# Kernel optimization log

Hardware: AMD Instinct MI355X
Metric: run time of the kernel (lower is better)

Reference implementation:

```python
import jax, jax.numpy as jnp
import numpy as np

B, D, H, E, W, R = 2048, 1024, 2048, 16, 4, 8
SCALE = 1.0


def setup_inputs() -> dict:
    key = jax.random.key(0)
    ks = jax.random.split(key, 10)
    s = 0.02
    return dict(
        z=jax.random.normal(ks[0], (B, D), jnp.float32),
        top_k=2,
        capacity=256,
        ban_expert=-1,
        tau=jnp.float32(1.0),
        epsilon=jnp.float32(0.0),
        fc1_w=jax.random.uniform(ks[1], (H, D), jnp.float32, -1.0, 1.0) / np.sqrt(D),
        fc1_b=jnp.zeros((H,), jnp.float32),
        fc2_w=jax.random.uniform(ks[2], (D, H), jnp.float32, -1.0, 1.0) / np.sqrt(H),
        fc2_b=jnp.zeros((D,), jnp.float32),
        prototypes=s * jax.random.normal(ks[3], (E, D), jnp.float32),
        adapter_keys=s * jax.random.normal(ks[4], (E, W, D), jnp.float32),
        expert_bias=jnp.zeros((E,), jnp.float32),
        a1=s * jax.random.normal(ks[5], (E, W, R, D), jnp.float32),
        b1=s * jax.random.normal(ks[6], (E, W, H, R), jnp.float32),
        a2=s * jax.random.normal(ks[7], (E, W, R, H), jnp.float32),
        b2=s * jax.random.normal(ks[8], (E, W, D, R), jnp.float32),
    )


def capacity_route(probs, top_k, capacity):
    # Greedy, order-dependent capacity-limited top-k routing (faithful to the
    # Python double loop): tokens processed in order, each takes its highest-
    # prob candidates whose expert still has free capacity.
    Bn, En = probs.shape
    k = min(top_k, En)
    cand_k = min(En, max(4 * k, k))
    cap_limit = max(1, capacity)
    vals, idxs = jax.lax.top_k(probs, cand_k)  # [B, cand_k]

    def token_step(cap, row):
        v_row, i_row = row

        def cand_step(st, x):
            slot, cap, a_idx, a_w, hit = st
            v, e, j = x
            take = (slot < k) & (cap[e] < cap_limit)
            s = jnp.minimum(slot, k - 1)
            a_idx = a_idx.at[s].set(jnp.where(take, e, a_idx[s]))
            a_w = a_w.at[s].set(jnp.where(take, v, a_w[s]))
            cap = cap.at[e].add(jnp.where(take, 1, 0).astype(cap.dtype))
            hit = hit + jnp.where(take & (j > 0), 1, 0)
            slot = slot + jnp.where(take, 1, 0)
            return (slot, cap, a_idx, a_w, hit), None

        init = (jnp.int32(0), cap,
                jnp.full((k,), -1, jnp.int32),
                jnp.zeros((k,), probs.dtype),
                jnp.int32(0))
        (slot, cap, a_idx, a_w, hit), _ = jax.lax.scan(
            cand_step, init, (v_row, i_row.astype(jnp.int32), jnp.arange(cand_k)))
        return cap, (a_idx, a_w, hit)

    cap0 = jnp.zeros((En,), jnp.int32)
    _, (assigned_idx, assigned_w, hits) = jax.lax.scan(token_step, cap0, (vals, idxs))
    cap_hit_rate = hits.sum().astype(probs.dtype) / max(1, Bn * k)
    return assigned_idx, assigned_w, cap_hit_rate


def reference(z, top_k, capacity, ban_expert, tau, epsilon,
              fc1_w, fc1_b, fc2_w, fc2_b, prototypes, adapter_keys,
              expert_bias, a1, b1, a2, b2):
    Bn = z.shape[0]
    En = prototypes.shape[0]
    h_pre = jax.nn.silu(z @ fc1_w.T + fc1_b)          # [B, H]
    out_pre = h_pre @ fc2_w.T + fc2_b                 # [B, D]

    logits = (z @ prototypes.T) / jnp.maximum(tau, 1e-6) + expert_bias
    logits = jnp.where(jnp.arange(En)[None, :] == ban_expert, -1e9, logits)
    probs = jax.nn.softmax(logits, axis=-1)
    probs = (1.0 - epsilon) * probs + epsilon / En

    assigned_idx, assigned_w, cap_hit_rate = capacity_route(probs, top_k, capacity)
    k = assigned_idx.shape[1]
    valid = assigned_idx >= 0                          # [B, k]
    e_safe = jnp.where(valid, assigned_idx, 0)         # [B, k]

    # adapter selection: argmax_w  z . adapter_keys[e, w]
    ak = adapter_keys[e_safe]                          # [B, k, W, D]
    a_idx = jnp.argmax(jnp.einsum('bd,bkwd->bkw', z, ak), axis=-1)  # [B, k]

    A1 = a1[e_safe, a_idx]                             # [B, k, R, D]
    B1 = b1[e_safe, a_idx]                             # [B, k, H, R]
    A2 = a2[e_safe, a_idx]                             # [B, k, R, H]
    B2 = b2[e_safe, a_idx]                             # [B, k, D, R]

    t1 = jnp.einsum('bd,bkrd->bkr', z, A1)
    d1 = jnp.einsum('bkr,bkhr->bkh', t1, B1) * SCALE
    h = jax.nn.silu(h_pre[:, None, :] + d1)            # [B, k, H]
    t2 = jnp.einsum('bkh,bkrh->bkr', h, A2)
    d2 = jnp.einsum('bkr,bkdr->bkd', t2, B2) * SCALE
    y = out_pre[:, None, :] + d2                       # [B, k, D]

    w = jnp.where(valid, assigned_w, 0.0)[:, :, None].astype(z.dtype)
    z_out = (w * y).sum(axis=1)                        # [B, D]

    used_mask = jnp.zeros((Bn, En), bool).at[jnp.arange(Bn)[:, None], e_safe].max(valid)
    # event lists, slot-major order, -1 marks unassigned slots (fixed shape for jit)
    ev_e = jnp.where(valid, assigned_idx, -1).T.reshape(-1)
    ev_a = jnp.where(valid, a_idx, -1).T.reshape(-1)

    return (z + z_out, probs, used_mask, assigned_idx, assigned_w,
            cap_hit_rate, ev_e, ev_a)
```

## Files before the change

### kernel.cpp

```cpp
#include <hip/hip_runtime.h>
#include <stdint.h>

#define NTOK 2048
#define DDIM 1024
#define HDIM 2048
#define NEXP 16

#define O_PROBS 2097152
#define O_USED  2129920
#define O_AIDX  2162688
#define O_AW    2166784
#define O_HIT   2170880
#define O_EVE   2170881
#define O_EVA   2174977

static constexpr size_t WS_ZBF    = 0;
static constexpr size_t WS_FC1WBF = WS_ZBF    + (size_t)NTOK * DDIM * 2;
static constexpr size_t WS_FC2WBF = WS_FC1WBF + (size_t)HDIM * DDIM * 2;
static constexpr size_t WS_HPREBF = WS_FC2WBF + (size_t)DDIM * HDIM * 2;
static constexpr size_t WS_OUTPRE = WS_HPREBF + (size_t)NTOK * HDIM * 2;
static constexpr size_t WS_A1BF   = WS_OUTPRE + (size_t)NTOK * DDIM * 4;
static constexpr size_t WS_B1BF   = WS_A1BF   + (size_t)16 * 4 * 8 * 1024 * 2;
static constexpr size_t WS_A2BF   = WS_B1BF   + (size_t)16 * 4 * 2048 * 8 * 2;
static constexpr size_t WS_B2BF   = WS_A2BF   + (size_t)16 * 4 * 8 * 2048 * 2;
static constexpr size_t WS_CANDS  = WS_B2BF   + (size_t)16 * 4 * 1024 * 8 * 2;
static constexpr size_t WS_CVALS  = WS_CANDS  + (size_t)NTOK * 4;
static constexpr size_t WS_ARGPK  = WS_CVALS  + (size_t)NTOK * 8 * 4;
static constexpr size_t WS_ASGN   = WS_ARGPK  + (size_t)NTOK * 4;
static constexpr size_t WS_ASGNW  = WS_ASGN   + (size_t)NTOK * 4;
static constexpr size_t WS_OUTPR2 = WS_ASGNW  + (size_t)NTOK * 2 * 4;
static constexpr size_t WS_TOTAL2 = WS_OUTPR2 + (size_t)NTOK * DDIM * 4;

typedef __bf16 v8bf __attribute__((ext_vector_type(8)));
typedef float v4f __attribute__((ext_vector_type(4)));
typedef unsigned short us8v __attribute__((ext_vector_type(8)));

__device__ __forceinline__ unsigned short f2bf(float f) {
  unsigned u = __float_as_uint(f);
  u = u + 0x7fffu + ((u >> 16) & 1u);
  return (unsigned short)(u >> 16);
}
__device__ __forceinline__ float bf2f(unsigned short s) {
  return __uint_as_float(((unsigned)s) << 16);
}
__device__ __forceinline__ void gload_lds16(const void* g, void* l) {
  __builtin_amdgcn_global_load_lds(
      (const __attribute__((address_space(1))) void*)g,
      (__attribute__((address_space(3))) void*)l, 16, 0, 0);
}
__device__ __forceinline__ float dot4(float4 a, float4 b) {
  return a.x * b.x + a.y * b.y + a.z * b.z + a.w * b.w;
}

__global__ __launch_bounds__(256) void k1_scores(
    const float* __restrict__ z, const float* __restrict__ proto,
    const float* __restrict__ ebias, const float* __restrict__ ak,
    const float* __restrict__ p_tau, const float* __restrict__ p_eps,
    const int* __restrict__ p_ban,
    unsigned short* __restrict__ zbf, float* __restrict__ out,
    unsigned* __restrict__ cands, float* __restrict__ cvals,
    unsigned* __restrict__ argpk,
    const float* __restrict__ fc1w, const float* __restrict__ fc2w,
    const float* __restrict__ a1, const float* __restrict__ b1,
    const float* __restrict__ a2, const float* __restrict__ b2,
    unsigned short* __restrict__ fc1wbf, unsigned short* __restrict__ fc2wbf,
    unsigned short* __restrict__ a1bf, unsigned short* __restrict__ b1bf,
    unsigned short* __restrict__ a2bf, unsigned short* __restrict__ b2bf)
{
  __shared__ float zs[4][DDIM];
  __shared__ float part[80 * 17];
  __shared__ float sc[4 * 80];
  const int tid = threadIdx.x;
  const int tb = blockIdx.x * 4;
#pragma unroll
  for (int i = 0; i < 4; ++i) {
    const int col = tid * 4;
    float4 v = *(const float4*)&z[(size_t)(tb + i) * DDIM + col];
    *(float4*)&zs[i][col] = v;
    ushort4 bv;
    bv.x = f2bf(v.x); bv.y = f2bf(v.y); bv.z = f2bf(v.z); bv.w = f2bf(v.w);
    *(ushort4*)&zbf[(size_t)(tb + i) * DDIM + col] = bv;
  }
  __syncthreads();
  const int wv = tid >> 6, l = tid & 63;

  {
    const float4* akr = (const float4*)(ak + (size_t)l * DDIM + wv * 256);
    const float4* z0 = (const float4*)&zs[0][0] + wv * 64;
    const float4* z1 = (const float4*)&zs[1][0] + wv * 64;
    const float4* z2 = (const float4*)&zs[2][0] + wv * 64;
    const float4* z3 = (const float4*)&zs[3][0] + wv * 64;
    float a0 = 0.f, a1v = 0.f, a2v = 0.f, a3 = 0.f;
#pragma unroll 8
    for (int i = 0; i < 64; ++i) {
      float4 w = akr[i];
      a0 += dot4(z0[i], w); a1v += dot4(z1[i], w);
      a2v += dot4(z2[i], w); a3 += dot4(z3[i], w);
    }
    part[l * 17 + 0 * 4 + wv] = a0;
    part[l * 17 + 1 * 4 + wv] = a1v;
    part[l * 17 + 2 * 4 + wv] = a2v;
    part[l * 17 + 3 * 4 + wv] = a3;
  }
  if (l < 16) {
    const float4* pr = (const float4*)(proto + (size_t)l * DDIM + wv * 256);
    const float4* z0 = (const float4*)&zs[0][0] + wv * 64;
    const float4* z1 = (const float4*)&zs[1][0] + wv * 64;
    const float4* z2 = (const float4*)&zs[2][0] + wv * 64;
    const float4* z3 = (const float4*)&zs[3][0] + wv * 64;
    float a0 = 0.f, a1v = 0.f, a2v = 0.f, a3 = 0.f;
#pragma unroll 8
    for (int i = 0; i < 64; ++i) {
      float4 w = pr[i];
      a0 += dot4(z0[i], w); a1v += dot4(z1[i], w);
      a2v += dot4(z2[i], w); a3 += dot4(z3[i], w);
    }
    part[(64 + l) * 17 + 0 * 4 + wv] = a0;
    part[(64 + l) * 17 + 1 * 4 + wv] = a1v;
    part[(64 + l) * 17 + 2 * 4 + wv] = a2v;
    part[(64 + l) * 17 + 3 * 4 + wv] = a3;
  }
  __syncthreads();
  for (int o = tid; o < 320; o += 256) {
    const int row = o >> 2, tk = o & 3;
    sc[tk * 80 + row] =
        ((part[row * 17 + tk * 4 + 0] + part[row * 17 + tk * 4 + 1]) +
         part[row * 17 + tk * 4 + 2]) + part[row * 17 + tk * 4 + 3];
  }
  __syncthreads();
  if (tid < 4) {
    const int t = tb + tid;
    const float tau = fmaxf(p_tau[0], 1e-6f);
    const float eps = p_eps[0];
    const int ban = p_ban[0];
    float lg[16];
#pragma unroll
    for (int e = 0; e < 16; ++e) {
      float v = sc[tid * 80 + 64 + e] / tau + ebias[e];
      lg[e] = (e == ban) ? -1e9f : v;
    }
    float mx = lg[0];
#pragma unroll
    for (int e = 1; e < 16; ++e) mx = fmaxf(mx, lg[e]);
    float ex[16]; float sm = 0.f;
#pragma unroll
    for (int e = 0; e < 16; ++e) { ex[e] = expf(lg[e] - mx); sm += ex[e]; }
    float p[16];
#pragma unroll
    for (int e = 0; e < 16; ++e) {
      p[e] = (1.f - eps) * (ex[e] / sm) + eps / (float)NEXP;
      out[O_PROBS + (size_t)t * NEXP + e] = p[e];
    }
    unsigned pack = 0, taken = 0;
#pragma unroll
    for (int r = 0; r < 8; ++r) {
      float bv = -1e30f; int bi = 0;
#pragma unroll
      for (int e = 0; e < 16; ++e) {
        const bool c = !((taken >> e) & 1u) && (p[e] > bv);
        bv = c ? p[e] : bv; bi = c ? e : bi;
      }
      taken |= 1u << bi;
      pack |= ((unsigned)bi) << (4 * r);
      cvals[(size_t)t * 8 + r] = bv;
    }
    cands[t] = pack;
    unsigned apk = 0;
#pragma unroll
    for (int e = 0; e < 16; ++e) {
      float b = sc[tid * 80 + e * 4]; int bi = 0;
#pragma unroll
      for (int w = 1; w < 4; ++w) {
        const float v = sc[tid * 80 + e * 4 + w];
        if (v > b) { b = v; bi = w; }
      }
      apk |= ((unsigned)bi) << (2 * e);
    }
    argpk[t] = apk;
  }
  size_t j = (size_t)blockIdx.x * 256 + tid;
  const size_t stride = (size_t)512 * 256;
  for (; j < 1835008ull; j += stride) {
    const float* src; unsigned short* dst; size_t off;
    if (j < 524288) { src = fc1w; dst = fc1wbf; off = j; }
    else if (j < 1048576) { src = fc2w; dst = fc2wbf; off = j - 524288; }
    else if (j < 1179648) { src = a1; dst = a1bf; off = j - 1048576; }
    else if (j < 1441792) { src = b1; dst = b1bf; off = j - 1179648; }
    else if (j < 1703936) { src = a2; dst = a2bf; off = j - 1441792; }
    else { src = b2; dst = b2bf; off = j - 1703936; }
    float4 v = *(const float4*)&src[off * 4];
    ushort4 bv;
    bv.x = f2bf(v.x); bv.y = f2bf(v.y); bv.z = f2bf(v.z); bv.w = f2bf(v.w);
    *(ushort4*)&dst[off * 4] = bv;
  }
}

__device__ __forceinline__ void route_decide(unsigned c, int avail,
                                             unsigned& m, int& dec) {
  unsigned flags = 0;
#pragma unroll
  for (int j = 0; j < 8; ++j) {
    const int e = (c >> (4 * j)) & 15;
    flags |= ((unsigned)(avail >> e) & 1u) << j;
  }
  const int pc = __popc(flags);
  const int sc = pc < 2 ? pc : 2;
  const int j0 = __ffs(flags) - 1;
  const int j1 = __ffs(flags & (flags - 1)) - 1;
  const int r0 = sc > 0 ? j0 : 0;
  const int r1 = sc > 1 ? j1 : 0;
  const int e0 = (c >> (4 * r0)) & 15;
  const int e1 = (c >> (4 * r1)) & 15;
  m = (sc > 0 ? (1u << e0) : 0u) | (sc > 1 ? (1u << e1) : 0u);
  dec = e0 | (e1 << 4) | (r0 << 8) | (r1 << 11) | (sc << 14);
}

struct RouterSm {
  unsigned long long bal[32][17];
  int cap[16], T[16];
  int avail, t0, tfin, done, hits;
};

__global__ __launch_bounds__(1024) void k2_router(
    const unsigned* __restrict__ cands, const float* __restrict__ cvals,
    const unsigned* __restrict__ argpk, const int* __restrict__ p_cap,
    float* __restrict__ out, int* __restrict__ asgn, float* __restrict__ asgnw)
{
  __shared__ RouterSm S;
  const int tid = threadIdx.x;
  const int w = tid >> 6, l = tid & 63;
  if (tid == 0) { S.avail = 0xFFFF; S.t0 = 0; S.done = 0; S.hits = 0; }
  if (tid < 16) S.cap[tid] = 0;
  const int capl = max(1, p_cap[0]);
  const unsigned cA = cands[tid], cB = cands[tid + 1024];
  const unsigned aA = argpk[tid], aB = argpk[tid + 1024];
  int hits = 0;
  __syncthreads();

  for (int round = 0; round < 20; ++round) {
    const int t0 = S.t0;
    const int avail = S.avail;
    unsigned mA = 0, mB = 0;
    int dA = 0, dB = 0;
    if (tid >= t0) route_decide(cA, avail, mA, dA);
    if (tid + 1024 >= t0) route_decide(cB, avail, mB, dB);
    if (w * 64 + 63 < t0) {
      if (l < 16) S.bal[w][l] = 0ull;
    } else {
      for (int av = avail; av; av &= av - 1) {
        const int e = __ffs(av) - 1;
        unsigned long long b = __ballot((mA >> e) & 1);
        if (l == e) S.bal[w][e] = b;
      }
    }
    if (w * 64 + 1024 + 63 < t0) {
      if (l < 16) S.bal[w + 16][l] = 0ull;
    } else {
      for (int av = avail; av; av &= av - 1) {
        const int e = __ffs(av) - 1;
        unsigned long long b = __ballot((mB >> e) & 1);
        if (l == e) S.bal[w + 16][e] = b;
      }
    }
    __syncthreads();
    unsigned long long bm = 0;
    const bool eav = (avail >> w) & 1;
    {
      int myT = 0x7FFFFFFF;
      if (eav) {
        int cnt = 0;
        if (l < 32) { bm = S.bal[l][w]; cnt = __popcll(bm); }
        int tot = cnt;
#pragma unroll
        for (int o = 32; o; o >>= 1) tot += __shfl_xor(tot, o, 64);
        const int rem = capl - S.cap[w];
        if (tot >= rem) {
          int incl = cnt;
#pragma unroll
          for (int o = 1; o < 32; o <<= 1) {
            int u = __shfl_up(incl, o, 64);
            if (l >= o) incl += u;
          }
          if (l < 32) {
            const int need = rem - (incl - cnt);
            if (need >= 1 && need <= cnt) {
              unsigned long long bb = bm;
              for (int i = 1; i < need; ++i) bb &= bb - 1;
              myT = l * 64 + (__ffsll((unsigned long long)bb) - 1);
            }
          }
#pragma unroll
          for (int o = 32; o; o >>= 1) myT = min(myT, __shfl_xor(myT, o, 64));
        }
      }
      if (l == 0) S.T[w] = myT;
    }
    __syncthreads();
    if (w == 0) {
      int v = (l < 16) ? S.T[l] : 0x7FFFFFFF;
      int ts = v;
#pragma unroll
      for (int o = 32; o; o >>= 1) ts = min(ts, __shfl_xor(ts, o, 64));
      const int done = (ts == 0x7FFFFFFF);
      const int tf = done ? (NTOK - 1) : ts;
      if (l == 0) { S.tfin = tf; S.done = done; S.t0 = tf + 1; }
      if (l < 16 && v == ts) atomicAnd(&S.avail, ~(1 << l));
    }
    __syncthreads();
    const int tfin = S.tfin;
    if (eav) {
      int c2 = 0;
      if (l < 32) {
        const int hi = tfin - l * 64;
        unsigned long long mk =
            (hi < 0) ? 0ull : (hi >= 63 ? ~0ull : ((1ull << (hi + 1)) - 1ull));
        c2 = __popcll(bm & mk);
      }
#pragma unroll
      for (int o = 32; o; o >>= 1) c2 += __shfl_xor(c2, o, 64);
      if (l == 0) S.cap[w] += c2;
    }
#pragma unroll
    for (int half = 0; half < 2; ++half) {
      const int t = tid + half * 1024;
      const int d = half ? dB : dA;
      const unsigned ap = half ? aB : aA;
      if (t < t0 || t > tfin) continue;
      const int e0 = d & 15, e1 = (d >> 4) & 15;
      const int r0 = (d >> 8) & 7, r1 = (d >> 11) & 7, sc = (d >> 14) & 3;
      const int a0 = (ap >> (2 * e0)) & 3, a1i = (ap >> (2 * e1)) & 3;
      asgn[t] = e0 | (e1 << 4) | (a0 << 8) | (a1i << 10) | (sc << 12);
      asgnw[t * 2 + 0] = sc > 0 ? cvals[(size_t)t * 8 + r0] : 0.f;
      asgnw[t * 2 + 1] = sc > 1 ? cvals[(size_t)t * 8 + r1] : 0.f;
      hits += (sc > 0 && r0 > 0) + (sc > 1 && r1 > 0);
    }
    __syncthreads();
    if (S.done) break;
  }
#pragma unroll
  for (int o = 32; o; o >>= 1) hits += __shfl_xor(hits, o, 64);
  if (l == 0) atomicAdd(&S.hits, hits);
  __syncthreads();
  if (tid == 0) out[O_HIT] = (float)S.hits / (float)(NTOK * 2);
}

template <int EPI>
__device__ __forceinline__ void gemm_body(
    unsigned short* As, unsigned short* Bs, int bid,
    const unsigned short* __restrict__ A, const unsigned short* __restrict__ Bm,
    const float* __restrict__ bias, void* __restrict__ Cout,
    int M, int N, int Kloop, int lda, int add_bias)
{
  const int tid = threadIdx.x;
  const int wv = tid >> 6, l = tid & 63;
  const int ntile = N >> 7;
  const int trow = (bid / ntile) << 7;
  const int tcol = (bid % ntile) << 7;
  const int wr = wv >> 1, wc = wv & 1;
  v4f acc[4][4];
#pragma unroll
  for (int m = 0; m < 4; ++m)
#pragma unroll
    for (int n = 0; n < 4; ++n) acc[m][n] = (v4f){0.f, 0.f, 0.f, 0.f};

  const int lrow8 = l >> 3;
  const int lcol8 = (l & 7) << 3;
  const unsigned short* gA = A + (size_t)trow * lda;
  const unsigned short* gB = Bm + (size_t)tcol * lda;
  const int fr = l & 15, kof = (l >> 4) << 3;

  for (int k0 = 0; k0 < Kloop; k0 += 64) {
    __syncthreads();
#pragma unroll
    for (int i = 0; i < 4; ++i) {
      const int s = (wv << 2) + i;
      gload_lds16(gA + (size_t)(s * 8 + lrow8) * lda + k0 + lcol8, &As[s * 512]);
      gload_lds16(gB + (size_t)(s * 8 + lrow8) * lda + k0 + lcol8, &Bs[s * 512]);
    }
    __syncthreads();
    v8bf af[4][2], bf[4][2];
#pragma unroll
    for (int m = 0; m < 4; ++m) {
      const int row = wr * 64 + m * 16 + fr;
      af[m][0] = *(const v8bf*)&As[row * 64 + kof];
      af[m][1] = *(const v8bf*)&As[row * 64 + 32 + kof];
    }
#pragma unroll
    for (int n = 0; n < 4; ++n) {
      const int row = wc * 64 + n * 16 + fr;
      bf[n][0] = *(const v8bf*)&Bs[row * 64 + kof];
      bf[n][1] = *(const v8bf*)&Bs[row * 64 + 32 + kof];
    }
#pragma unroll
    for (int ks = 0; ks < 2; ++ks)
#pragma unroll
      for (int m = 0; m < 4; ++m)
#pragma unroll
        for (int n = 0; n < 4; ++n)
          acc[m][n] = __builtin_amdgcn_mfma_f32_16x16x32_bf16(
              af[m][ks], bf[n][ks], acc[m][n], 0, 0, 0);
  }
  const int fq = l >> 4;
#pragma unroll
  for (int m = 0; m < 4; ++m)
#pragma unroll
    for (int n = 0; n < 4; ++n) {
      const int col = tcol + wc * 64 + n * 16 + fr;
      const float bc = add_bias ? bias[col] : 0.f;
#pragma unroll
      for (int j = 0; j < 4; ++j) {
        const int row = trow + wr * 64 + m * 16 + fq * 4 + j;
        const float v = acc[m][n][j] + bc;
        if (EPI == 0) {
          const float sv = v / (1.f + __expf(-v));
          ((unsigned short*)Cout)[(size_t)row * N + col] = f2bf(sv);
        } else {
          ((float*)Cout)[(size_t)row * N + col] = v;
        }
      }
    }
}

__global__ __launch_bounds__(256) void gemm_bt0(
    const unsigned short* __restrict__ A, const unsigned short* __restrict__ Bm,
    const float* __restrict__ bias, void* __restrict__ Cout,
    int M, int N, int K)
{
  __shared__ __align__(16) char smem[32768];
  gemm_body<0>((unsigned short*)smem, (unsigned short*)smem + 8192,
               blockIdx.x, A, Bm, bias, Cout, M, N, K, K, 1);
}

__global__ __launch_bounds__(256) void gemm_bt1s(
    const unsigned short* __restrict__ A, const unsigned short* __restrict__ Bm,
    const float* __restrict__ bias, float* __restrict__ C0,
    float* __restrict__ C1)
{
  __shared__ __align__(16) char smem[32768];
  const int ntiles = (NTOK / 128) * (DDIM / 128);
  const int half = blockIdx.x / ntiles;
  const int tile = blockIdx.x % ntiles;
  gemm_body<1>((unsigned short*)smem, (unsigned short*)smem + 8192,
               tile, A + half * 1024, Bm + half * 1024, bias,
               half ? (void*)C1 : (void*)C0,
               NTOK, DDIM, 1024, HDIM, half == 0);
}

__global__ __launch_bounds__(256) void gemm_bt1f(
    const unsigned short* __restrict__ A, const unsigned short* __restrict__ Bm,
    const float* __restrict__ bias, void* __restrict__ Cout,
    int M, int N, int K)
{
  __shared__ __align__(16) char smem[32768];
  gemm_body<1>((unsigned short*)smem, (unsigned short*)smem + 8192,
               blockIdx.x, A, Bm, bias, Cout, M, N, K, K, 1);
}

__global__ __launch_bounds__(256) void k5_lora(
    const float* __restrict__ z, const unsigned short* __restrict__ hpre,
    const float* __restrict__ outpre, const float* __restrict__ outpre2,
    int use2, const int* __restrict__ asgn, const float* __restrict__ asgnw,
    const unsigned short* __restrict__ a1, const unsigned short* __restrict__ b1,
    const unsigned short* __restrict__ a2, const unsigned short* __restrict__ b2,
    float* __restrict__ out0, float* __restrict__ out)
{
  __shared__ float zl[DDIM];
  __shared__ float hl[HDIM];
  __shared__ float t1s[8], t2s[8];
  const int b = blockIdx.x, tid = threadIdx.x;
  {
    float4 v = *(const float4*)&z[(size_t)b * DDIM + tid * 4];
    *(float4*)&zl[tid * 4] = v;
  }
  const int pk = asgn[b];
  const int sc = (pk >> 12) & 3;
  const int eA0 = pk & 15, eA1 = (pk >> 4) & 15;
  const int aA0 = (pk >> 8) & 3, aA1 = (pk >> 10) & 3;
  const float w0 = asgnw[b * 2 + 0], w1 = asgnw[b * 2 + 1];
  if (tid < 16)
    out[O_USED + (size_t)b * 16 + tid] =
        (float)((sc > 0 && tid == eA0) || (sc > 1 && tid == eA1));
  if (tid == 0) {
    out[O_AIDX + (size_t)b * 2 + 0] = sc > 0 ? (float)eA0 : -1.f;
    out[O_AIDX + (size_t)b * 2 + 1] = sc > 1 ? (float)eA1 : -1.f;
    out[O_AW + (size_t)b * 2 + 0] = w0;
    out[O_AW + (size_t)b * 2 + 1] = w1;
    out[O_EVE + b] = sc > 0 ? (float)eA0 : -1.f;
    out[O_EVE + NTOK + b] = sc > 1 ? (float)eA1 : -1.f;
    out[O_EVA + b] = sc > 0 ? (float)aA0 : -1.f;
    out[O_EVA + NTOK + b] = sc > 1 ? (float)aA1 : -1.f;
  }
  float acc[4] = {0.f, 0.f, 0.f, 0.f};
  float wsum = 0.f;
  const int r = tid >> 5, l5 = tid & 31;
  const float4* zg = (const float4*)&z[(size_t)b * DDIM];
  __syncthreads();

  for (int s = 0; s < 2; ++s) {
    if (s >= sc) continue;
    const float ww = (s == 0) ? w0 : w1;
    const int ad = ((s == 0) ? eA0 : eA1) * 4 + ((s == 0) ? aA0 : aA1);
    wsum += ww;
    {
      const us8v* pa1 = (const us8v*)(a1 + ((size_t)ad * 8 + r) * DDIM);
      float sa = 0.f;
#pragma unroll
      for (int i = 0; i < 4; ++i) {
        const int g = l5 + 32 * i;
        us8v va = pa1[g];
        float4 z0 = zg[g * 2], z1 = zg[g * 2 + 1];
        sa += z0.x * bf2f(va[0]) + z0.y * bf2f(va[1]) +
              z0.z * bf2f(va[2]) + z0.w * bf2f(va[3]) +
              z1.x * bf2f(va[4]) + z1.y * bf2f(va[5]) +
              z1.z * bf2f(va[6]) + z1.w * bf2f(va[7]);
      }
#pragma unroll
      for (int o = 16; o; o >>= 1) sa += __shfl_xor(sa, o, 64);
      if (l5 == 0) t1s[r] = sa;
    }
    __syncthreads();
    {
      float t1r[8];
#pragma unroll
      for (int q = 0; q < 8; ++q) t1r[q] = t1s[q];
      const unsigned short* pb1 = b1 + (size_t)ad * HDIM * 8;
      const unsigned short* ph = hpre + (size_t)b * HDIM;
#pragma unroll
      for (int j = 0; j < 8; ++j) {
        const int hh_i = tid + 256 * j;
        us8v row = *(const us8v*)&pb1[(size_t)hh_i * 8];
        float d1 = 0.f;
#pragma unroll
        for (int q = 0; q < 8; ++q) d1 += t1r[q] * bf2f(row[q]);
        const float hh = bf2f(ph[hh_i]) + d1;
        hl[hh_i] = hh / (1.f + __expf(-hh));
      }
    }
    __syncthreads();
    {
      const us8v* pa2 = (const us8v*)(a2 + ((size_t)ad * 8 + r) * HDIM);
      float sa = 0.f;
#pragma unroll
      for (int i = 0; i < 8; ++i) {
        const int g = l5 + 32 * i;
        us8v va = pa2[g];
        const float* hp = &hl[g * 8];
        sa += hp[0] * bf2f(va[0]) + hp[1] * bf2f(va[1]) +
              hp[2] * bf2f(va[2]) + hp[3] * bf2f(va[3]) +
              hp[4] * bf2f(va[4]) + hp[5] * bf2f(va[5]) +
              hp[6] * bf2f(va[6]) + hp[7] * bf2f(va[7]);
      }
#pragma unroll
      for (int o = 16; o; o >>= 1) sa += __shfl_xor(sa, o, 64);
      if (l5 == 0) t2s[r] = sa;
    }
    __syncthreads();
    {
      float t2r[8];
#pragma unroll
      for (int q = 0; q < 8; ++q) t2r[q] = t2s[q];
      const unsigned short* pb2 = b2 + (size_t)ad * DDIM * 8;
#pragma unroll
      for (int j = 0; j < 4; ++j) {
        const int d = tid + 256 * j;
        us8v row = *(const us8v*)&pb2[(size_t)d * 8];
        float d2 = 0.f;
#pragma unroll
        for (int q = 0; q < 8; ++q) d2 += t2r[q] * bf2f(row[q]);
        acc[j] += ww * d2;
      }
    }
    __syncthreads();
  }
#pragma unroll
  for (int j = 0; j < 4; ++j) {
    const int d = tid + 256 * j;
    float op = outpre[(size_t)b * DDIM + d];
    if (use2) op += outpre2[(size_t)b * DDIM + d];
    out0[(size_t)b * DDIM + d] = zl[d] + wsum * op + acc[j];
  }
}

extern "C" void kernel_launch(void* const* d_in, const int* in_sizes, int n_in,
                              void* d_out, int out_size, void* d_ws, size_t ws_size,
                              hipStream_t stream)
{
  (void)in_sizes; (void)n_in; (void)out_size;
  const float* z     = (const float*)d_in[0];
  const int*   p_cap = (const int*)d_in[2];
  const int*   p_ban = (const int*)d_in[3];
  const float* p_tau = (const float*)d_in[4];
  const float* p_eps = (const float*)d_in[5];
  const float* fc1w  = (const float*)d_in[6];
  const float* fc1b  = (const float*)d_in[7];
  const float* fc2w  = (const float*)d_in[8];
  const float* fc2b  = (const float*)d_in[9];
  const float* proto = (const float*)d_in[10];
  const float* ak    = (const float*)d_in[11];
  const float* ebias = (const float*)d_in[12];
  const float* a1    = (const float*)d_in[13];
  const float* b1    = (const float*)d_in[14];
  const float* a2    = (const float*)d_in[15];
  const float* b2    = (const float*)d_in[16];
  float* out = (float*)d_out;
  char* ws = (char*)d_ws;

  unsigned short* zbf    = (unsigned short*)(ws + WS_ZBF);
  unsigned short* fc1wbf = (unsigned short*)(ws + WS_FC1WBF);
  unsigned short* fc2wbf = (unsigned short*)(ws + WS_FC2WBF);
  unsigned short* hprebf = (unsigned short*)(ws + WS_HPREBF);
  float*          outpre = (float*)(ws + WS_OUTPRE);
  unsigned short* a1bf   = (unsigned short*)(ws + WS_A1BF);
  unsigned short* b1bf   = (unsigned short*)(ws + WS_B1BF);
  unsigned short* a2bf   = (unsigned short*)(ws + WS_A2BF);
  unsigned short* b2bf   = (unsigned short*)(ws + WS_B2BF);
  unsigned*       cands  = (unsigned*)(ws + WS_CANDS);
  float*          cvals  = (float*)(ws + WS_CVALS);
  unsigned*       argpk  = (unsigned*)(ws + WS_ARGPK);
  int*            asgn   = (int*)(ws + WS_ASGN);
  float*          asgnw  = (float*)(ws + WS_ASGNW);
  float*          outpr2 = (float*)(ws + WS_OUTPR2);
  const int splitk = (ws_size >= WS_TOTAL2) ? 1 : 0;

  k1_scores<<<512, 256, 0, stream>>>(
      z, proto, ebias, ak, p_tau, p_eps, p_ban, zbf, out, cands, cvals, argpk,
      fc1w, fc2w, a1, b1, a2, b2, fc1wbf, fc2wbf, a1bf, b1bf, a2bf, b2bf);

  k2_router<<<1, 1024, 0, stream>>>(
      cands, cvals, argpk, p_cap, out, asgn, asgnw);

  gemm_bt0<<<(NTOK / 128) * (HDIM / 128), 256, 0, stream>>>(
      zbf, fc1wbf, fc1b, (void*)hprebf, NTOK, HDIM, DDIM);

  if (splitk) {
    gemm_bt1s<<<2 * (NTOK / 128) * (DDIM / 128), 256, 0, stream>>>(
        hprebf, fc2wbf, fc2b, outpre, outpr2);
  } else {
    gemm_bt1f<<<(NTOK / 128) * (DDIM / 128), 256, 0, stream>>>(
        hprebf, fc2wbf, fc2b, (void*)outpre, NTOK, DDIM, HDIM);
  }

  k5_lora<<<NTOK, 256, 0, stream>>>(
      z, hprebf, outpre, outpr2, splitk, asgn, asgnw,
      a1bf, b1bf, a2bf, b2bf, out, out);
}
```

Measured before the change: 279.5 us.

## Overlap weight bf16 conversion with serial router and trim router barriers

Moves the fp32-to-bf16 conversion of the fc and LoRA weights out of the scoring kernel into extra blocks of the single-block router launch, so the conversion runs on otherwise idle CUs while the serial routing loop executes. The router itself keeps capacity, avail and t0 in registers, double-buffers the ballot array, and drops one barrier per round by having every wave compute the min threshold redundantly. It also preloads candidate values into registers. The risk is that the conversion blocks contend for memory bandwidth with the router block, and the conversion loop now runs with a different block count.

```diff
diff --git a/kernel.cpp b/kernel.cpp
--- a/kernel.cpp
+++ b/kernel.cpp
@@ -59,13 +59,7 @@
     const int* __restrict__ p_ban,
     unsigned short* __restrict__ zbf, float* __restrict__ out,
     unsigned* __restrict__ cands, float* __restrict__ cvals,
-    unsigned* __restrict__ argpk,
-    const float* __restrict__ fc1w, const float* __restrict__ fc2w,
-    const float* __restrict__ a1, const float* __restrict__ b1,
-    const float* __restrict__ a2, const float* __restrict__ b2,
-    unsigned short* __restrict__ fc1wbf, unsigned short* __restrict__ fc2wbf,
-    unsigned short* __restrict__ a1bf, unsigned short* __restrict__ b1bf,
-    unsigned short* __restrict__ a2bf, unsigned short* __restrict__ b2bf)
+    unsigned* __restrict__ argpk)
 {
   __shared__ float zs[4][DDIM];
   __shared__ float part[80 * 17];
@@ -178,22 +172,9 @@
     }
     argpk[t] = apk;
   }
-  size_t j = (size_t)blockIdx.x * 256 + tid;
-  const size_t stride = (size_t)512 * 256;
-  for (; j < 1835008ull; j += stride) {
-    const float* src; unsigned short* dst; size_t off;
-    if (j < 524288) { src = fc1w; dst = fc1wbf; off = j; }
-    else if (j < 1048576) { src = fc2w; dst = fc2wbf; off = j - 524288; }
-    else if (j < 1179648) { src = a1; dst = a1bf; off = j - 1048576; }
-    else if (j < 1441792) { src = b1; dst = b1bf; off = j - 1179648; }
-    else if (j < 1703936) { src = a2; dst = a2bf; off = j - 1441792; }
-    else { src = b2; dst = b2bf; off = j - 1703936; }
-    float4 v = *(const float4*)&src[off * 4];
-    ushort4 bv;
-    bv.x = f2bf(v.x); bv.y = f2bf(v.y); bv.z = f2bf(v.z); bv.w = f2bf(v.w);
-    *(ushort4*)&dst[off * 4] = bv;
-  }
-}
+}
+
+#define CONVB 224
 
 __device__ __forceinline__ void route_decide(unsigned c, int avail,
                                              unsigned& m, int& dec) {
@@ -215,99 +196,107 @@
   dec = e0 | (e1 << 4) | (r0 << 8) | (r1 << 11) | (sc << 14);
 }
 
-struct RouterSm {
-  unsigned long long bal[32][17];
-  int cap[16], T[16];
-  int avail, t0, tfin, done, hits;
-};
-
-__global__ __launch_bounds__(1024) void k2_router(
+__global__ __launch_bounds__(1024) void k2_route_conv(
     const unsigned* __restrict__ cands, const float* __restrict__ cvals,
     const unsigned* __restrict__ argpk, const int* __restrict__ p_cap,
-    float* __restrict__ out, int* __restrict__ asgn, float* __restrict__ asgnw)
-{
-  __shared__ RouterSm S;
+    float* __restrict__ out, int* __restrict__ asgn, float* __restrict__ asgnw,
+    const float* __restrict__ fc1w, const float* __restrict__ fc2w,
+    const float* __restrict__ a1, const float* __restrict__ b1,
+    const float* __restrict__ a2, const float* __restrict__ b2,
+    unsigned short* __restrict__ fc1wbf, unsigned short* __restrict__ fc2wbf,
+    unsigned short* __restrict__ a1bf, unsigned short* __restrict__ b1bf,
+    unsigned short* __restrict__ a2bf, unsigned short* __restrict__ b2bf)
+{
   const int tid = threadIdx.x;
+  if (blockIdx.x != 0) {
+    size_t j = (size_t)(blockIdx.x - 1) * 1024 + tid;
+    const size_t stride = (size_t)CONVB * 1024;
+    for (; j < 1835008ull; j += stride) {
+      const float* src; unsigned short* dst; size_t off;
+      if (j < 524288) { src = fc1w; dst = fc1wbf; off = j; }
+      else if (j < 1048576) { src = fc2w; dst = fc2wbf; off = j - 524288; }
+      else if (j < 1179648) { src = a1; dst = a1bf; off = j - 1048576; }
+      else if (j < 1441792) { src = b1; dst = b1bf; off = j - 1179648; }
+      else if (j < 1703936) { src = a2; dst = a2bf; off = j - 1441792; }
+      else { src = b2; dst = b2bf; off = j - 1703936; }
+      float4 v = *(const float4*)&src[off * 4];
+      ushort4 bv;
+      bv.x = f2bf(v.x); bv.y = f2bf(v.y); bv.z = f2bf(v.z); bv.w = f2bf(v.w);
+      *(ushort4*)&dst[off * 4] = bv;
+    }
+    return;
+  }
+  __shared__ unsigned long long bal[2][32][17];
+  __shared__ int T[16];
+  __shared__ int hitsS;
   const int w = tid >> 6, l = tid & 63;
-  if (tid == 0) { S.avail = 0xFFFF; S.t0 = 0; S.done = 0; S.hits = 0; }
-  if (tid < 16) S.cap[tid] = 0;
+  if (tid == 0) hitsS = 0;
   const int capl = max(1, p_cap[0]);
   const unsigned cA = cands[tid], cB = cands[tid + 1024];
   const unsigned aA = argpk[tid], aB = argpk[tid + 1024];
-  int hits = 0;
-  __syncthreads();
+  float cvA[8], cvB[8];
+#pragma unroll
+  for (int q = 0; q < 8; ++q) {
+    cvA[q] = cvals[(size_t)tid * 8 + q];
+    cvB[q] = cvals[(size_t)(tid + 1024) * 8 + q];
+  }
+  int avail = 0xFFFF, t0 = 0, capw = 0, hits = 0;
 
   for (int round = 0; round < 20; ++round) {
-    const int t0 = S.t0;
-    const int avail = S.avail;
+    const int p = round & 1;
     unsigned mA = 0, mB = 0;
     int dA = 0, dB = 0;
     if (tid >= t0) route_decide(cA, avail, mA, dA);
     if (tid + 1024 >= t0) route_decide(cB, avail, mB, dB);
-    if (w * 64 + 63 < t0) {
-      if (l < 16) S.bal[w][l] = 0ull;
-    } else {
-      for (int av = avail; av; av &= av - 1) {
-        const int e = __ffs(av) - 1;
-        unsigned long long b = __ballot((mA >> e) & 1);
-        if (l == e) S.bal[w][e] = b;
-      }
-    }
-    if (w * 64 + 1024 + 63 < t0) {
-      if (l < 16) S.bal[w + 16][l] = 0ull;
-    } else {
-      for (int av = avail; av; av &= av - 1) {
-        const int e = __ffs(av) - 1;
-        unsigned long long b = __ballot((mB >> e) & 1);
-        if (l == e) S.bal[w + 16][e] = b;
-      }
+#pragma unroll
+    for (int e = 0; e < 16; ++e) {
+      unsigned long long b = __ballot((mA >> e) & 1);
+      if (l == e) bal[p][w][l] = b;
+    }
+#pragma unroll
+    for (int e = 0; e < 16; ++e) {
+      unsigned long long b = __ballot((mB >> e) & 1);
+      if (l == e) bal[p][w + 16][l] = b;
     }
     __syncthreads();
     unsigned long long bm = 0;
+    int myT = 0x7FFFFFFF;
     const bool eav = (avail >> w) & 1;
-    {
-      int myT = 0x7FFFFFFF;
-      if (eav) {
-        int cnt = 0;
-        if (l < 32) { bm = S.bal[l][w]; cnt = __popcll(bm); }
-        int tot = cnt;
-#pragma unroll
-        for (int o = 32; o; o >>= 1) tot += __shfl_xor(tot, o, 64);
-        const int rem = capl - S.cap[w];
-        if (tot >= rem) {
-          int incl = cnt;
-#pragma unroll
-          for (int o = 1; o < 32; o <<= 1) {
-            int u = __shfl_up(incl, o, 64);
-            if (l >= o) incl += u;
+    if (eav) {
+      int cnt = 0;
+      if (l < 32) { bm = bal[p][l][w]; cnt = __popcll(bm); }
+      int tot = cnt;
+#pragma unroll
+      for (int o = 32; o; o >>= 1) tot += __shfl_xor(tot, o, 64);
+      const int rem = capl - capw;
+      if (tot >= rem) {
+        int incl = cnt;
+#pragma unroll
+        for (int o = 1; o < 32; o <<= 1) {
+          int u = __shfl_up(incl, o, 64);
+          if (l >= o) incl += u;
+        }
+        if (l < 32) {
+          const int need = rem - (incl - cnt);
+          if (need >= 1 && need <= cnt) {
+            unsigned long long bb = bm;
+            for (int i = 1; i < need; ++i) bb &= bb - 1;
+            myT = l * 64 + (__ffsll((unsigned long long)bb) - 1);
           }
-          if (l < 32) {
-            const int need = rem - (incl - cnt);
-            if (need >= 1 && need <= cnt) {
-              unsigned long long bb = bm;
-              for (int i = 1; i < need; ++i) bb &= bb - 1;
-              myT = l * 64 + (__ffsll((unsigned long long)bb) - 1);
-            }
-          }
-#pragma unroll
-          for (int o = 32; o; o >>= 1) myT = min(myT, __shfl_xor(myT, o, 64));
         }
-      }
-      if (l == 0) S.T[w] = myT;
-    }
-    __syncthreads();
-    if (w == 0) {
-      int v = (l < 16) ? S.T[l] : 0x7FFFFFFF;
-      int ts = v;
-#pragma unroll
-      for (int o = 32; o; o >>= 1) ts = min(ts, __shfl_xor(ts, o, 64));
-      const int done = (ts == 0x7FFFFFFF);
-      const int tf = done ? (NTOK - 1) : ts;
-      if (l == 0) { S.tfin = tf; S.done = done; S.t0 = tf + 1; }
-      if (l < 16 && v == ts) atomicAnd(&S.avail, ~(1 << l));
-    }
-    __syncthreads();
-    const int tfin = S.tfin;
+#pragma unroll
+        for (int o = 32; o; o >>= 1) myT = min(myT, __shfl_xor(myT, o, 64));
+      }
+    }
+    if (l == 0) T[w] = myT;
+    __syncthreads();
+    const int tv = (l < 16) ? T[l] : 0x7FFFFFFF;
+    int ts = tv;
+#pragma unroll
+    for (int o = 32; o; o >>= 1) ts = min(ts, __shfl_xor(ts, o, 64));
+    const bool done = (ts == 0x7FFFFFFF);
+    const int tfin = done ? (NTOK - 1) : ts;
+    unsigned long long crossed = __ballot((l < 16) && !done && (tv == ts));
     if (eav) {
       int c2 = 0;
       if (l < 32) {
@@ -318,30 +307,53 @@
       }
 #pragma unroll
       for (int o = 32; o; o >>= 1) c2 += __shfl_xor(c2, o, 64);
-      if (l == 0) S.cap[w] += c2;
-    }
-#pragma unroll
-    for (int half = 0; half < 2; ++half) {
-      const int t = tid + half * 1024;
-      const int d = half ? dB : dA;
-      const unsigned ap = half ? aB : aA;
-      if (t < t0 || t > tfin) continue;
-      const int e0 = d & 15, e1 = (d >> 4) & 15;
-      const int r0 = (d >> 8) & 7, r1 = (d >> 11) & 7, sc = (d >> 14) & 3;
-      const int a0 = (ap >> (2 * e0)) & 3, a1i = (ap >> (2 * e1)) & 3;
-      asgn[t] = e0 | (e1 << 4) | (a0 << 8) | (a1i << 10) | (sc << 12);
-      asgnw[t * 2 + 0] = sc > 0 ? cvals[(size_t)t * 8 + r0] : 0.f;
-      asgnw[t * 2 + 1] = sc > 1 ? cvals[(size_t)t * 8 + r1] : 0.f;
-      hits += (sc > 0 && r0 > 0) + (sc > 1 && r1 > 0);
-    }
-    __syncthreads();
-    if (S.done) break;
+      capw += c2;
+    }
+    {
+      const int t = tid;
+      if (t >= t0 && t <= tfin) {
+        const int e0 = dA & 15, e1 = (dA >> 4) & 15;
+        const int r0 = (dA >> 8) & 7, r1 = (dA >> 11) & 7, sc = (dA >> 14) & 3;
+        const int a0 = (aA >> (2 * e0)) & 3, a1i = (aA >> (2 * e1)) & 3;
+        float w0 = 0.f, w1v = 0.f;
+#pragma unroll
+        for (int q = 0; q < 8; ++q) {
+          if (q == r0) w0 = cvA[q];
+          if (q == r1) w1v = cvA[q];
+        }
+        asgn[t] = e0 | (e1 << 4) | (a0 << 8) | (a1i << 10) | (sc << 12);
+        asgnw[t * 2 + 0] = sc > 0 ? w0 : 0.f;
+        asgnw[t * 2 + 1] = sc > 1 ? w1v : 0.f;
+        hits += (sc > 0 && r0 > 0) + (sc > 1 && r1 > 0);
+      }
+    }
+    {
+      const int t = tid + 1024;
+      if (t >= t0 && t <= tfin) {
+        const int e0 = dB & 15, e1 = (dB >> 4) & 15;
+        const int r0 = (dB >> 8) & 7, r1 = (dB >> 11) & 7, sc = (dB >> 14) & 3;
+        const int a0 = (aB >> (2 * e0)) & 3, a1i = (aB >> (2 * e1)) & 3;
+        float w0 = 0.f, w1v = 0.f;
+#pragma unroll
+        for (int q = 0; q < 8; ++q) {
+          if (q == r0) w0 = cvB[q];
+          if (q == r1) w1v = cvB[q];
+        }
+        asgn[t] = e0 | (e1 << 4) | (a0 << 8) | (a1i << 10) | (sc << 12);
+        asgnw[t * 2 + 0] = sc > 0 ? w0 : 0.f;
+        asgnw[t * 2 + 1] = sc > 1 ? w1v : 0.f;
+        hits += (sc > 0 && r0 > 0) + (sc > 1 && r1 > 0);
+      }
+    }
+    avail &= ~(int)(unsigned)(crossed & 0xFFFFull);
+    t0 = tfin + 1;
+    if (done) break;
   }
 #pragma unroll
   for (int o = 32; o; o >>= 1) hits += __shfl_xor(hits, o, 64);
-  if (l == 0) atomicAdd(&S.hits, hits);
+  if (l == 0) atomicAdd(&hitsS, hits);
   __syncthreads();
-  if (tid == 0) out[O_HIT] = (float)S.hits / (float)(NTOK * 2);
+  if (tid == 0) out[O_HIT] = (float)hitsS / (float)(NTOK * 2);
 }
 
 template <int EPI>
@@ -623,11 +635,12 @@
   const int splitk = (ws_size >= WS_TOTAL2) ? 1 : 0;
 
   k1_scores<<<512, 256, 0, stream>>>(
-      z, proto, ebias, ak, p_tau, p_eps, p_ban, zbf, out, cands, cvals, argpk,
-      fc1w, fc2w, a1, b1, a2, b2, fc1wbf, fc2wbf, a1bf, b1bf, a2bf, b2bf);
-
-  k2_router<<<1, 1024, 0, stream>>>(
-      cands, cvals, argpk, p_cap, out, asgn, asgnw);
+      z, proto, ebias, ak, p_tau, p_eps, p_ban, zbf, out, cands, cvals, argpk);
+
+  k2_route_conv<<<1 + CONVB, 1024, 0, stream>>>(
+      cands, cvals, argpk, p_cap, out, asgn, asgnw,
+      fc1w, fc2w, a1, b1, a2, b2,
+      fc1wbf, fc2wbf, a1bf, b1bf, a2bf, b2bf);
 
   gemm_bt0<<<(NTOK / 128) * (HDIM / 128), 256, 0, stream>>>(
       zbf, fc1wbf, fc1b, (void*)hprebf, NTOK, HDIM, DDIM);
```

Result: faster. 272.8 us (-2.4%).
